# Performance work log

Measured on AMD Instinct MI355X. Metric: run time of the kernel, lower is better.

The kernel has to match this reference:

```python
import jax, jax.numpy as jnp
import numpy as np

B, S, H, E, I_E, V = 4, 4096, 1024, 8, 512, 100000


def setup_inputs() -> dict:
    key = jax.random.key(0)
    k0, k1, k2, k3, k4, k5, k6 = jax.random.split(key, 7)
    hidden_states = jax.random.normal(k0, (B, S, H), dtype=jnp.float32)
    token_ids = jax.random.randint(k1, (B, S), 0, V, dtype=jnp.int64)
    mu = jax.random.normal(k2, (B, S, H), dtype=jnp.float32)
    # torch Linear(in,out,bias=False) weight is [out,in]; we store transposed [in,out]
    w_gate = jax.random.normal(k3, (E, H, I_E), dtype=jnp.float32) * 0.02
    w_up = jax.random.normal(k4, (E, H, I_E), dtype=jnp.float32) * 0.02
    w_down = jax.random.normal(k5, (E, I_E, H), dtype=jnp.float32) * 0.02
    # module zero-inits mu_router; use small random so the mu-override path is exercised
    mu_router_w = jax.random.normal(k6, (E, H), dtype=jnp.float32) * 0.02
    return {
        "hidden_states": hidden_states,
        "token_ids": token_ids,
        "mu": mu,
        "w_gate": w_gate,
        "w_up": w_up,
        "w_down": w_down,
        "mu_router_w": mu_router_w,
    }


def reference(hidden_states, token_ids, mu, w_gate, w_up, w_down, mu_router_w):
    num_experts = w_gate.shape[0]
    # deterministic token->expert mapping: token_id % num_experts (after clamp)
    tid = jnp.clip(token_ids, 0, V - 1)
    base_expert_ids = (tid % num_experts).astype(jnp.int32)  # [B,S]
    # mu-guided override: one_hot*10 + mu_logits, argmax
    mu_logits = jnp.einsum("bsh,eh->bse", mu, mu_router_w)
    base_one_hot = jax.nn.one_hot(base_expert_ids, num_experts, dtype=mu_logits.dtype)
    expert_ids = jnp.argmax(base_one_hot * 10.0 + mu_logits, axis=-1)  # [B,S]

    x = hidden_states.reshape(-1, H)          # [T,H], T=B*S
    eid = expert_ids.reshape(-1)              # [T]
    out = jnp.zeros_like(x)
    for e in range(num_experts):
        mask = (eid == e)[:, None]            # [T,1]
        g = x @ w_gate[e]                     # [T,I_E]
        u = x @ w_up[e]                       # [T,I_E]
        y = (jax.nn.silu(g) * u) @ w_down[e]  # [T,H] SwiGLU
        out = out + jnp.where(mask, y, 0.0)
    return out.reshape(hidden_states.shape)
```

## Files before the change

kernel.cpp:

```cpp
#include <hip/hip_runtime.h>
#include <stdint.h>

#define T_TOK   16384
#define H_DIM   1024
#define IE_DIM  512
#define E_NUM   8
#define V_MAX   100000

typedef __attribute__((ext_vector_type(8))) short bf16x8;
typedef __attribute__((ext_vector_type(4))) float f32x4;
typedef unsigned long long ull;

__device__ __forceinline__ unsigned short f2bf(float f) {
  union { float f; unsigned u; } v; v.f = f;
  unsigned r = v.u + 0x7fffu + ((v.u >> 16) & 1u);
  return (unsigned short)(r >> 16);
}

__device__ __forceinline__ void gload16(const void* g, void* l) {
  __builtin_amdgcn_global_load_lds(
      (const __attribute__((address_space(1))) unsigned int*)g,
      (__attribute__((address_space(3))) unsigned int*)(unsigned int)(uintptr_t)l,
      16, 0, 0);
}

__global__ __launch_bounds__(256) void k_pre(
    const float* __restrict__ mu, const int* __restrict__ tok,
    const float* __restrict__ mrw, int* __restrict__ eid,
    int* __restrict__ blockCnt,
    const float* __restrict__ wg, const float* __restrict__ wu,
    const float* __restrict__ wd, unsigned short* __restrict__ WgT,
    unsigned short* __restrict__ WuT, unsigned short* __restrict__ WdT) {
  __shared__ unsigned short lds[64][72];
  int tid = threadIdx.x;

  if (blockIdx.x < 1024) {
    int* cnt = (int*)&lds[0][0];
    if (tid < 8) cnt[tid] = 0;
    int wv = blockIdx.x * 4 + (tid >> 6);
    int t0 = wv * 4;
    int lane = tid & 63;
    const float4* mrw4 = (const float4*)mrw;

    float acc[4][E_NUM];
#pragma unroll
    for (int i = 0; i < 4; i++)
#pragma unroll
      for (int e = 0; e < E_NUM; e++) acc[i][e] = 0.f;

#pragma unroll
    for (int j = 0; j < 4; j++) {
      int idx = lane + 64 * j;
      float4 wr[E_NUM];
#pragma unroll
      for (int e = 0; e < E_NUM; e++) wr[e] = mrw4[e * 256 + idx];
#pragma unroll
      for (int i = 0; i < 4; i++) {
        float4 m = ((const float4*)(mu + (size_t)(t0 + i) * H_DIM))[idx];
#pragma unroll
        for (int e = 0; e < E_NUM; e++)
          acc[i][e] += m.x * wr[e].x + m.y * wr[e].y + m.z * wr[e].z + m.w * wr[e].w;
      }
    }
#pragma unroll
    for (int i = 0; i < 4; i++)
#pragma unroll
      for (int e = 0; e < E_NUM; e++)
#pragma unroll
        for (int off = 32; off >= 1; off >>= 1)
          acc[i][e] += __shfl_xor(acc[i][e], off, 64);

    __syncthreads();
#pragma unroll
    for (int i = 0; i < 4; i++) {
      int tv = tok[t0 + i];
      if (tv < 0) tv = 0;
      if (tv > V_MAX - 1) tv = V_MAX - 1;
      int base = tv & 7;
      int best = 0; float bs = -1e30f;
#pragma unroll
      for (int e = 0; e < E_NUM; e++) {
        float s = acc[i][e] + (e == base ? 10.f : 0.f);
        if (s > bs) { bs = s; best = e; }
      }
      if (lane == i) {
        eid[t0 + i] = best;
        atomicAdd(&cnt[best], 1);
      }
    }
    __syncthreads();
    if (tid < 8) blockCnt[blockIdx.x * 8 + tid] = cnt[tid];
  } else {
    int sel = (blockIdx.x - 1024) >> 10;
    int blk = blockIdx.x & 1023;
    const float* src; unsigned short* dst; int R, C;
    if (sel == 0)      { src = wg; dst = WgT; R = H_DIM; C = IE_DIM; }
    else if (sel == 1) { src = wu; dst = WuT; R = H_DIM; C = IE_DIM; }
    else               { src = wd; dst = WdT; R = IE_DIM; C = H_DIM; }
    int tpe = (R >> 6) * (C >> 6);
    int e = blk / tpe;
    int rem = blk % tpe;
    int tr = rem / (C >> 6);
    int tc = rem % (C >> 6);
    const float* s = src + (size_t)e * R * C;
    unsigned short* d = dst + (size_t)e * R * C;
    int r0 = tid >> 4;
    int c0 = (tid & 15) * 4;
#pragma unroll
    for (int i = 0; i < 4; i++) {
      int r = r0 + i * 16;
      float4 v = *(const float4*)(s + (size_t)(tr * 64 + r) * C + tc * 64 + c0);
      lds[r][c0 + 0] = f2bf(v.x); lds[r][c0 + 1] = f2bf(v.y);
      lds[r][c0 + 2] = f2bf(v.z); lds[r][c0 + 3] = f2bf(v.w);
    }
    __syncthreads();
    int oc = tid >> 2;
    int ob = (tid & 3) * 16;
    unsigned short tmp[16];
#pragma unroll
    for (int i = 0; i < 16; i++) tmp[i] = lds[ob + i][oc];
    uint4* dp = (uint4*)(d + (size_t)(tc * 64 + oc) * R + tr * 64 + ob);
    dp[0] = ((uint4*)tmp)[0];
    dp[1] = ((uint4*)tmp)[1];
  }
}

__global__ __launch_bounds__(1024) void k_scan2(
    const int* __restrict__ blockCnt, int* __restrict__ blockBase,
    int* __restrict__ offsets, int* __restrict__ tileOff) {
  int b = threadIdx.x;
  __shared__ ull s0[1024], s1[1024];
  __shared__ int offL[8];
  const int4* p = (const int4*)(blockCnt + b * 8);
  int4 x0 = p[0], x1 = p[1];
  int c[8] = {x0.x, x0.y, x0.z, x0.w, x1.x, x1.y, x1.z, x1.w};
  ull v0 = (ull)c[0] | ((ull)c[1] << 16) | ((ull)c[2] << 32) | ((ull)c[3] << 48);
  ull v1 = (ull)c[4] | ((ull)c[5] << 16) | ((ull)c[6] << 32) | ((ull)c[7] << 48);
  s0[b] = v0; s1[b] = v1;
  __syncthreads();
  for (int st = 1; st < 1024; st <<= 1) {
    ull a0 = 0, a1 = 0;
    if (b >= st) { a0 = s0[b - st]; a1 = s1[b - st]; }
    __syncthreads();
    v0 += a0; v1 += a1;
    s0[b] = v0; s1[b] = v1;
    __syncthreads();
  }
  if (b == 1023) {
    int tot[8];
#pragma unroll
    for (int e = 0; e < 4; e++) tot[e] = (int)((v0 >> (16 * e)) & 0xFFFF);
#pragma unroll
    for (int e = 0; e < 4; e++) tot[4 + e] = (int)((v1 >> (16 * e)) & 0xFFFF);
    int s = 0, ts = 0;
    for (int e = 0; e < E_NUM; e++) {
      offsets[e] = s; offL[e] = s; tileOff[e] = ts;
      s += tot[e];
      ts += (tot[e] + 127) >> 7;
    }
    offsets[E_NUM] = s; tileOff[E_NUM] = ts;
  }
  __syncthreads();
  int be[8];
#pragma unroll
  for (int e = 0; e < 4; e++)
    be[e] = offL[e] + (int)((v0 >> (16 * e)) & 0xFFFF) - c[e];
#pragma unroll
  for (int e = 0; e < 4; e++)
    be[4 + e] = offL[4 + e] + (int)((v1 >> (16 * e)) & 0xFFFF) - c[4 + e];
  int4* q = (int4*)(blockBase + b * 8);
  q[0] = make_int4(be[0], be[1], be[2], be[3]);
  q[1] = make_int4(be[4], be[5], be[6], be[7]);
}

__global__ __launch_bounds__(256) void k_gather(
    const float* __restrict__ hs, const int* __restrict__ eid,
    const int* __restrict__ blockBase, int* __restrict__ tokofrow,
    unsigned short* __restrict__ Xs) {
  int b = blockIdx.x;
  int tid = threadIdx.x;
  __shared__ int eL[16];
  __shared__ int posL[16];
  if (tid < 16) eL[tid] = eid[b * 16 + tid];
  __syncthreads();
  if (tid < 16) {
    int e = eL[tid];
    int r = 0;
    for (int j = 0; j < tid; j++) r += (eL[j] == e);
    int pos = blockBase[b * 8 + e] + r;
    posL[tid] = pos;
    tokofrow[pos] = b * 16 + tid;
  }
  __syncthreads();
  int w = tid >> 6, lane = tid & 63;
#pragma unroll
  for (int i = 0; i < 4; i++) {
    int li = w * 4 + i;
    int t = b * 16 + li;
    int pos = posL[li];
    const float4* src = (const float4*)(hs + (size_t)t * H_DIM);
    unsigned short* drow = Xs + (size_t)pos * H_DIM;
#pragma unroll
    for (int j = 0; j < 4; j++) {
      float4 v = src[lane + 64 * j];
      ushort4 bb;
      bb.x = f2bf(v.x); bb.y = f2bf(v.y); bb.z = f2bf(v.z); bb.w = f2bf(v.w);
      *(ushort4*)(drow + (lane + 64 * j) * 4) = bb;
    }
  }
}

__global__ __launch_bounds__(512) void k_gemm1(
    const unsigned short* __restrict__ Xs,
    const unsigned short* __restrict__ WgT,
    const unsigned short* __restrict__ WuT,
    unsigned short* __restrict__ Hb,
    const int* __restrict__ offsets, const int* __restrict__ tileOff) {
  int bid0 = blockIdx.x;
  int xcd = bid0 & 7, seq = bid0 >> 3;
  int wg = (xcd < 4 ? xcd * 68 : 272 + (xcd - 4) * 67) + seq;
  int nt = wg & 3;
  int mlin = wg >> 2;
  if (mlin >= tileOff[E_NUM]) return;
  int e = 0;
#pragma unroll
  for (int i = 1; i < E_NUM; i++)
    if (mlin >= tileOff[i]) e = i;
  int mtile = mlin - tileOff[e];
  int segStart = offsets[e], segEnd = offsets[e + 1];
  int M = segEnd - segStart;

  __shared__ unsigned short Alds[3][128 * 32];
  __shared__ unsigned short Bglds[3][128 * 32];
  __shared__ unsigned short Bulds[3][128 * 32];

  int tid = threadIdx.x;
  int lane = tid & 63;
  int w = tid >> 6;
  int wm = w >> 2;
  int wn = w & 3;

  f32x4 accg[4][2], accu[4][2];
#pragma unroll
  for (int i = 0; i < 4; i++)
#pragma unroll
    for (int j = 0; j < 2; j++) {
      accg[i][j] = (f32x4)(0.f);
      accu[i][j] = (f32x4)(0.f);
    }

  int sr = tid >> 2;
  int sc = tid & 3;
  int scc = sc ^ ((sr >> 1) & 3);
  int grow = mtile * 128 + sr;
  if (grow > M - 1) grow = M - 1;
  const unsigned short* Arow = Xs + (size_t)(segStart + grow) * H_DIM + scc * 8;
  const unsigned short* Bgrow =
      WgT + (size_t)e * IE_DIM * H_DIM + (size_t)(nt * 128 + sr) * H_DIM + scc * 8;
  const unsigned short* Burow =
      WuT + (size_t)e * IE_DIM * H_DIM + (size_t)(nt * 128 + sr) * H_DIM + scc * 8;

#define STAGE1(buf, k0)                                            \
  {                                                                \
    gload16(Arow + (k0), (char*)Alds[buf] + tid * 16);             \
    gload16(Bgrow + (k0), (char*)Bglds[buf] + tid * 16);           \
    gload16(Burow + (k0), (char*)Bulds[buf] + tid * 16);           \
  }

  int kc = lane >> 4;
  int arow[4], browv[2];
#pragma unroll
  for (int mf = 0; mf < 4; mf++) arow[mf] = wm * 64 + mf * 16 + (lane & 15);
#pragma unroll
  for (int nf = 0; nf < 2; nf++) browv[nf] = wn * 32 + nf * 16 + (lane & 15);

  const int NT = H_DIM / 32;
  STAGE1(0, 0);
  STAGE1(1, 32);

  int cur = 0;
  for (int t = 0; t < NT; t++) {
    asm volatile("s_waitcnt vmcnt(3)" ::: "memory");
    __builtin_amdgcn_s_barrier();
    __builtin_amdgcn_sched_barrier(0);
    int tn = t + 2; if (tn >= NT) tn -= NT;
    int nbuf = cur + 2; if (nbuf >= 3) nbuf -= 3;
    STAGE1(nbuf, tn * 32);

    bf16x8 a[4], bg[2], bu[2];
#pragma unroll
    for (int mf = 0; mf < 4; mf++) {
      int row = arow[mf];
      int byte = row * 64 + ((kc ^ ((row >> 1) & 3)) << 4);
      a[mf] = *(const bf16x8*)((const char*)Alds[cur] + byte);
    }
#pragma unroll
    for (int nf = 0; nf < 2; nf++) {
      int row = browv[nf];
      int byte = row * 64 + ((kc ^ ((row >> 1) & 3)) << 4);
      bg[nf] = *(const bf16x8*)((const char*)Bglds[cur] + byte);
      bu[nf] = *(const bf16x8*)((const char*)Bulds[cur] + byte);
    }
    __builtin_amdgcn_s_setprio(1);
#pragma unroll
    for (int mf = 0; mf < 4; mf++)
#pragma unroll
      for (int nf = 0; nf < 2; nf++) {
        accg[mf][nf] = __builtin_amdgcn_mfma_f32_16x16x32_bf16(
            a[mf], bg[nf], accg[mf][nf], 0, 0, 0);
        accu[mf][nf] = __builtin_amdgcn_mfma_f32_16x16x32_bf16(
            a[mf], bu[nf], accu[mf][nf], 0, 0, 0);
      }
    __builtin_amdgcn_s_setprio(0);
    cur = (cur + 1 == 3) ? 0 : cur + 1;
  }
#undef STAGE1
  asm volatile("s_waitcnt vmcnt(0)" ::: "memory");

  int rowBase = segStart + mtile * 128 + wm * 64;
#pragma unroll
  for (int mf = 0; mf < 4; mf++)
#pragma unroll
    for (int nf = 0; nf < 2; nf++) {
      int col = nt * 128 + wn * 32 + nf * 16 + (lane & 15);
#pragma unroll
      for (int j = 0; j < 4; j++) {
        int r = rowBase + mf * 16 + (lane >> 4) * 4 + j;
        if (r < segEnd) {
          float g = accg[mf][nf][j];
          float u = accu[mf][nf][j];
          float h = (g / (1.f + __expf(-g))) * u;
          Hb[(size_t)r * IE_DIM + col] = f2bf(h);
        }
      }
    }
}

__global__ __launch_bounds__(512) void k_gemm2(
    const unsigned short* __restrict__ Hb,
    const unsigned short* __restrict__ WdT,
    float* __restrict__ out,
    const int* __restrict__ offsets, const int* __restrict__ tileOff,
    const int* __restrict__ tokofrow) {
  int bid0 = blockIdx.x;
  int wg = (bid0 & 7) * 135 + (bid0 >> 3);
  int nt = wg & 7;
  int mlin = wg >> 3;
  if (mlin >= tileOff[E_NUM]) return;
  int e = 0;
#pragma unroll
  for (int i = 1; i < E_NUM; i++)
    if (mlin >= tileOff[i]) e = i;
  int mtile = mlin - tileOff[e];
  int segStart = offsets[e], segEnd = offsets[e + 1];
  int M = segEnd - segStart;

  __shared__ unsigned short Alds[3][128 * 32];
  __shared__ unsigned short Blds[3][128 * 32];

  int tid = threadIdx.x;
  int lane = tid & 63;
  int w = tid >> 6;
  int wm = w >> 2;
  int wn = w & 3;

  f32x4 acc[4][2];
#pragma unroll
  for (int i = 0; i < 4; i++)
#pragma unroll
    for (int j = 0; j < 2; j++) acc[i][j] = (f32x4)(0.f);

  int sr = tid >> 2;
  int sc = tid & 3;
  int scc = sc ^ ((sr >> 1) & 3);
  int grow = mtile * 128 + sr;
  if (grow > M - 1) grow = M - 1;
  const unsigned short* Arow = Hb + (size_t)(segStart + grow) * IE_DIM + scc * 8;
  const unsigned short* Brow =
      WdT + (size_t)e * H_DIM * IE_DIM + (size_t)(nt * 128 + sr) * IE_DIM + scc * 8;

#define STAGE2(buf, k0)                                            \
  {                                                                \
    gload16(Arow + (k0), (char*)Alds[buf] + tid * 16);             \
    gload16(Brow + (k0), (char*)Blds[buf] + tid * 16);             \
  }

  int kc = lane >> 4;
  int arow[4], browv[2];
#pragma unroll
  for (int mf = 0; mf < 4; mf++) arow[mf] = wm * 64 + mf * 16 + (lane & 15);
#pragma unroll
  for (int nf = 0; nf < 2; nf++) browv[nf] = wn * 32 + nf * 16 + (lane & 15);

  const int NT = IE_DIM / 32;
  STAGE2(0, 0);
  STAGE2(1, 32);

  int cur = 0;
  for (int t = 0; t < NT; t++) {
    asm volatile("s_waitcnt vmcnt(2)" ::: "memory");
    __builtin_amdgcn_s_barrier();
    __builtin_amdgcn_sched_barrier(0);
    int tn = t + 2; if (tn >= NT) tn -= NT;
    int nbuf = cur + 2; if (nbuf >= 3) nbuf -= 3;
    STAGE2(nbuf, tn * 32);

    bf16x8 a[4], b[2];
#pragma unroll
    for (int mf = 0; mf < 4; mf++) {
      int row = arow[mf];
      int byte = row * 64 + ((kc ^ ((row >> 1) & 3)) << 4);
      a[mf] = *(const bf16x8*)((const char*)Alds[cur] + byte);
    }
#pragma unroll
    for (int nf = 0; nf < 2; nf++) {
      int row = browv[nf];
      int byte = row * 64 + ((kc ^ ((row >> 1) & 3)) << 4);
      b[nf] = *(const bf16x8*)((const char*)Blds[cur] + byte);
    }
    __builtin_amdgcn_s_setprio(1);
#pragma unroll
    for (int mf = 0; mf < 4; mf++)
#pragma unroll
      for (int nf = 0; nf < 2; nf++)
        acc[mf][nf] = __builtin_amdgcn_mfma_f32_16x16x32_bf16(
            a[mf], b[nf], acc[mf][nf], 0, 0, 0);
    __builtin_amdgcn_s_setprio(0);
    cur = (cur + 1 == 3) ? 0 : cur + 1;
  }
#undef STAGE2
  asm volatile("s_waitcnt vmcnt(0)" ::: "memory");

  int rowBase = segStart + mtile * 128 + wm * 64;
#pragma unroll
  for (int mf = 0; mf < 4; mf++)
#pragma unroll
    for (int nf = 0; nf < 2; nf++) {
      int col = nt * 128 + wn * 32 + nf * 16 + (lane & 15);
#pragma unroll
      for (int j = 0; j < 4; j++) {
        int r = rowBase + mf * 16 + (lane >> 4) * 4 + j;
        if (r < segEnd) {
          int t = tokofrow[r];
          out[(size_t)t * H_DIM + col] = acc[mf][nf][j];
        }
      }
    }
}

#define WS_XS    ((size_t)0)
#define WS_WGT   ((size_t)33554432)
#define WS_WUT   ((size_t)41943040)
#define WS_WDT   ((size_t)50331648)
#define WS_HB    ((size_t)58720256)
#define WS_EID   ((size_t)75497472)
#define WS_TOK   ((size_t)75563008)
#define WS_OFF   ((size_t)75628544)
#define WS_BC    ((size_t)75629568)
#define WS_BB    ((size_t)75662336)

extern "C" void kernel_launch(void* const* d_in, const int* in_sizes, int n_in,
                              void* d_out, int out_size, void* d_ws, size_t ws_size,
                              hipStream_t stream) {
  const float* hs  = (const float*)d_in[0];
  const int*   tok = (const int*)d_in[1];
  const float* mu  = (const float*)d_in[2];
  const float* wg  = (const float*)d_in[3];
  const float* wu  = (const float*)d_in[4];
  const float* wd  = (const float*)d_in[5];
  const float* mrw = (const float*)d_in[6];
  float* out = (float*)d_out;
  char* ws = (char*)d_ws;

  unsigned short* Xs  = (unsigned short*)(ws + WS_XS);
  unsigned short* WgT = (unsigned short*)(ws + WS_WGT);
  unsigned short* WuT = (unsigned short*)(ws + WS_WUT);
  unsigned short* WdT = (unsigned short*)(ws + WS_WDT);
  unsigned short* Hb  = (unsigned short*)(ws + WS_HB);
  int* eid      = (int*)(ws + WS_EID);
  int* tokofrow = (int*)(ws + WS_TOK);
  int* offsets  = (int*)(ws + WS_OFF);
  int* tileOff  = offsets + 16;
  int* blockCnt = (int*)(ws + WS_BC);
  int* blockBase= (int*)(ws + WS_BB);

  k_pre<<<4096, 256, 0, stream>>>(mu, tok, mrw, eid, blockCnt,
                                  wg, wu, wd, WgT, WuT, WdT);
  k_scan2<<<1, 1024, 0, stream>>>(blockCnt, blockBase, offsets, tileOff);
  k_gather<<<1024, 256, 0, stream>>>(hs, eid, blockBase, tokofrow, Xs);
  k_gemm1<<<135 * 4, 512, 0, stream>>>(Xs, WgT, WuT, Hb, offsets, tileOff);
  k_gemm2<<<135 * 8, 512, 0, stream>>>(Hb, WdT, out, offsets, tileOff, tokofrow);
}
```

Measured before the change: 155.8 us.

## Enlarge gemm1 tiles to 256x128 with K=64 double-buffered staging

Rewrites the fused gate/up GEMM kernel to use 256-row M tiles and a 64-wide K step with two LDS buffers instead of three 32-wide ones. Each wave now computes a 64x64 block for both gate and up, which raises MFMA work per LDS load and halves the loop trip count. The scan kernel now emits separate 256-row tile offsets for gemm1 and 128-row offsets for gemm2, and the XCD remapping and grid size are adjusted to match. The cost is much higher register and LDS use, so occupancy drops to one block per CU. Fewer blocks also means more padding waste on partial expert tiles.

```diff
diff --git a/kernel.cpp b/kernel.cpp
--- a/kernel.cpp
+++ b/kernel.cpp
@@ -127,7 +127,8 @@
 
 __global__ __launch_bounds__(1024) void k_scan2(
     const int* __restrict__ blockCnt, int* __restrict__ blockBase,
-    int* __restrict__ offsets, int* __restrict__ tileOff) {
+    int* __restrict__ offsets, int* __restrict__ tileOff,
+    int* __restrict__ tileOff128) {
   int b = threadIdx.x;
   __shared__ ull s0[1024], s1[1024];
   __shared__ int offL[8];
@@ -152,13 +153,15 @@
     for (int e = 0; e < 4; e++) tot[e] = (int)((v0 >> (16 * e)) & 0xFFFF);
 #pragma unroll
     for (int e = 0; e < 4; e++) tot[4 + e] = (int)((v1 >> (16 * e)) & 0xFFFF);
-    int s = 0, ts = 0;
+    int s = 0, ts = 0, ts2 = 0;
     for (int e = 0; e < E_NUM; e++) {
-      offsets[e] = s; offL[e] = s; tileOff[e] = ts;
+      offsets[e] = s; offL[e] = s;
+      tileOff[e] = ts; tileOff128[e] = ts2;
       s += tot[e];
-      ts += (tot[e] + 127) >> 7;
-    }
-    offsets[E_NUM] = s; tileOff[E_NUM] = ts;
+      ts += (tot[e] + 255) >> 8;
+      ts2 += (tot[e] + 127) >> 7;
+    }
+    offsets[E_NUM] = s; tileOff[E_NUM] = ts; tileOff128[E_NUM] = ts2;
   }
   __syncthreads();
   int be[8];
@@ -210,7 +213,7 @@
   }
 }
 
-__global__ __launch_bounds__(512) void k_gemm1(
+__global__ __launch_bounds__(512, 1) void k_gemm1(
     const unsigned short* __restrict__ Xs,
     const unsigned short* __restrict__ WgT,
     const unsigned short* __restrict__ WuT,
@@ -218,7 +221,7 @@
     const int* __restrict__ offsets, const int* __restrict__ tileOff) {
   int bid0 = blockIdx.x;
   int xcd = bid0 & 7, seq = bid0 >> 3;
-  int wg = (xcd < 4 ? xcd * 68 : 272 + (xcd - 4) * 67) + seq;
+  int wg = (xcd < 4 ? xcd * 36 : 144 + (xcd - 4) * 35) + seq;
   int nt = wg & 3;
   int mlin = wg >> 2;
   if (mlin >= tileOff[E_NUM]) return;
@@ -230,99 +233,171 @@
   int segStart = offsets[e], segEnd = offsets[e + 1];
   int M = segEnd - segStart;
 
-  __shared__ unsigned short Alds[3][128 * 32];
-  __shared__ unsigned short Bglds[3][128 * 32];
-  __shared__ unsigned short Bulds[3][128 * 32];
+  __shared__ unsigned short Alds[2][256 * 64];
+  __shared__ unsigned short Bglds[2][128 * 64];
+  __shared__ unsigned short Bulds[2][128 * 64];
 
   int tid = threadIdx.x;
   int lane = tid & 63;
   int w = tid >> 6;
-  int wm = w >> 2;
-  int wn = w & 3;
-
-  f32x4 accg[4][2], accu[4][2];
+  int wm = w >> 1;
+  int wn = w & 1;
+  int r0 = lane & 15;
+  int kcb = lane >> 4;
+
+  f32x4 accg[4][4], accu[4][4];
 #pragma unroll
   for (int i = 0; i < 4; i++)
 #pragma unroll
-    for (int j = 0; j < 2; j++) {
+    for (int j = 0; j < 4; j++) {
       accg[i][j] = (f32x4)(0.f);
       accu[i][j] = (f32x4)(0.f);
     }
 
-  int sr = tid >> 2;
-  int sc = tid & 3;
-  int scc = sc ^ ((sr >> 1) & 3);
-  int grow = mtile * 128 + sr;
-  if (grow > M - 1) grow = M - 1;
-  const unsigned short* Arow = Xs + (size_t)(segStart + grow) * H_DIM + scc * 8;
-  const unsigned short* Bgrow =
-      WgT + (size_t)e * IE_DIM * H_DIM + (size_t)(nt * 128 + sr) * H_DIM + scc * 8;
-  const unsigned short* Burow =
-      WuT + (size_t)e * IE_DIM * H_DIM + (size_t)(nt * 128 + sr) * H_DIM + scc * 8;
-
-#define STAGE1(buf, k0)                                            \
-  {                                                                \
-    gload16(Arow + (k0), (char*)Alds[buf] + tid * 16);             \
-    gload16(Bgrow + (k0), (char*)Bglds[buf] + tid * 16);           \
-    gload16(Burow + (k0), (char*)Bulds[buf] + tid * 16);           \
-  }
-
-  int kc = lane >> 4;
-  int arow[4], browv[2];
-#pragma unroll
-  for (int mf = 0; mf < 4; mf++) arow[mf] = wm * 64 + mf * 16 + (lane & 15);
-#pragma unroll
-  for (int nf = 0; nf < 2; nf++) browv[nf] = wn * 32 + nf * 16 + (lane & 15);
-
-  const int NT = H_DIM / 32;
-  STAGE1(0, 0);
-  STAGE1(1, 32);
-
-  int cur = 0;
-  for (int t = 0; t < NT; t++) {
-    asm volatile("s_waitcnt vmcnt(3)" ::: "memory");
+  const unsigned short* Asrc[4];
+#pragma unroll
+  for (int i = 0; i < 4; i++) {
+    int s = tid + i * 512;
+    int row = s >> 3;
+    int ch = (s & 7) ^ (row & 7);
+    int gr = mtile * 256 + row; if (gr > M - 1) gr = M - 1;
+    Asrc[i] = Xs + (size_t)(segStart + gr) * H_DIM + ch * 8;
+  }
+  const unsigned short* Bgsrc[2];
+  const unsigned short* Busrc[2];
+#pragma unroll
+  for (int i = 0; i < 2; i++) {
+    int s = tid + i * 512;
+    int row = s >> 3;
+    int ch = (s & 7) ^ (row & 7);
+    Bgsrc[i] = WgT + (size_t)e * IE_DIM * H_DIM + (size_t)(nt * 128 + row) * H_DIM + ch * 8;
+    Busrc[i] = WuT + (size_t)e * IE_DIM * H_DIM + (size_t)(nt * 128 + row) * H_DIM + ch * 8;
+  }
+
+#define GLA(i, kt, buf) gload16(Asrc[i] + (kt) * 64, (char*)Alds[buf] + (tid + (i) * 512) * 16)
+#define GLG(i, kt, buf) gload16(Bgsrc[i] + (kt) * 64, (char*)Bglds[buf] + (tid + (i) * 512) * 16)
+#define GLU(i, kt, buf) gload16(Busrc[i] + (kt) * 64, (char*)Bulds[buf] + (tid + (i) * 512) * 16)
+
+  int aoff[4][2], boff[4][2];
+#pragma unroll
+  for (int mf = 0; mf < 4; mf++) {
+    int row = wm * 64 + mf * 16 + r0;
+#pragma unroll
+    for (int ks = 0; ks < 2; ks++) {
+      int c = ks * 4 + kcb;
+      aoff[mf][ks] = row * 128 + ((c ^ (row & 7)) << 4);
+    }
+  }
+#pragma unroll
+  for (int nf = 0; nf < 4; nf++) {
+    int row = wn * 64 + nf * 16 + r0;
+#pragma unroll
+    for (int ks = 0; ks < 2; ks++) {
+      int c = ks * 4 + kcb;
+      boff[nf][ks] = row * 128 + ((c ^ (row & 7)) << 4);
+    }
+  }
+
+  const int NT = H_DIM / 64;
+  GLA(0, 0, 0); GLA(1, 0, 0); GLA(2, 0, 0); GLA(3, 0, 0);
+  GLG(0, 0, 0); GLG(1, 0, 0); GLU(0, 0, 0); GLU(1, 0, 0);
+
+  bf16x8 a0[2][2], a1[2][2], bb[4][2];
+
+  for (int kt = 0; kt < NT; kt++) {
+    int buf = kt & 1, nbuf = buf ^ 1;
+    int ktn = (kt + 1 < NT) ? kt + 1 : 0;
+    const char* Ab = (const char*)Alds[buf];
+    const char* Bgb = (const char*)Bglds[buf];
+    const char* Bub = (const char*)Bulds[buf];
+
     __builtin_amdgcn_s_barrier();
+    GLA(0, ktn, nbuf); GLA(1, ktn, nbuf); GLA(2, ktn, nbuf); GLA(3, ktn, nbuf);
+    GLG(0, ktn, nbuf); GLG(1, ktn, nbuf); GLU(0, ktn, nbuf); GLU(1, ktn, nbuf);
+    asm volatile("s_waitcnt vmcnt(8)" ::: "memory");
+    __builtin_amdgcn_s_barrier();
+
+#pragma unroll
+    for (int mf = 0; mf < 2; mf++)
+#pragma unroll
+      for (int ks = 0; ks < 2; ks++)
+        a0[mf][ks] = *(const bf16x8*)(Ab + aoff[mf][ks]);
+#pragma unroll
+    for (int nf = 0; nf < 4; nf++)
+#pragma unroll
+      for (int ks = 0; ks < 2; ks++)
+        bb[nf][ks] = *(const bf16x8*)(Bgb + boff[nf][ks]);
+    asm volatile("s_waitcnt lgkmcnt(0)" ::: "memory");
     __builtin_amdgcn_sched_barrier(0);
-    int tn = t + 2; if (tn >= NT) tn -= NT;
-    int nbuf = cur + 2; if (nbuf >= 3) nbuf -= 3;
-    STAGE1(nbuf, tn * 32);
-
-    bf16x8 a[4], bg[2], bu[2];
-#pragma unroll
-    for (int mf = 0; mf < 4; mf++) {
-      int row = arow[mf];
-      int byte = row * 64 + ((kc ^ ((row >> 1) & 3)) << 4);
-      a[mf] = *(const bf16x8*)((const char*)Alds[cur] + byte);
-    }
-#pragma unroll
-    for (int nf = 0; nf < 2; nf++) {
-      int row = browv[nf];
-      int byte = row * 64 + ((kc ^ ((row >> 1) & 3)) << 4);
-      bg[nf] = *(const bf16x8*)((const char*)Bglds[cur] + byte);
-      bu[nf] = *(const bf16x8*)((const char*)Bulds[cur] + byte);
-    }
     __builtin_amdgcn_s_setprio(1);
 #pragma unroll
-    for (int mf = 0; mf < 4; mf++)
-#pragma unroll
-      for (int nf = 0; nf < 2; nf++) {
-        accg[mf][nf] = __builtin_amdgcn_mfma_f32_16x16x32_bf16(
-            a[mf], bg[nf], accg[mf][nf], 0, 0, 0);
-        accu[mf][nf] = __builtin_amdgcn_mfma_f32_16x16x32_bf16(
-            a[mf], bu[nf], accu[mf][nf], 0, 0, 0);
-      }
+    for (int mf = 0; mf < 2; mf++)
+#pragma unroll
+      for (int nf = 0; nf < 4; nf++)
+#pragma unroll
+        for (int ks = 0; ks < 2; ks++)
+          accg[mf][nf] = __builtin_amdgcn_mfma_f32_16x16x32_bf16(
+              a0[mf][ks], bb[nf][ks], accg[mf][nf], 0, 0, 0);
     __builtin_amdgcn_s_setprio(0);
-    cur = (cur + 1 == 3) ? 0 : cur + 1;
-  }
-#undef STAGE1
+
+#pragma unroll
+    for (int mf = 0; mf < 2; mf++)
+#pragma unroll
+      for (int ks = 0; ks < 2; ks++)
+        a1[mf][ks] = *(const bf16x8*)(Ab + aoff[2 + mf][ks]);
+    asm volatile("s_waitcnt lgkmcnt(0)" ::: "memory");
+    __builtin_amdgcn_sched_barrier(0);
+    __builtin_amdgcn_s_setprio(1);
+#pragma unroll
+    for (int mf = 0; mf < 2; mf++)
+#pragma unroll
+      for (int nf = 0; nf < 4; nf++)
+#pragma unroll
+        for (int ks = 0; ks < 2; ks++)
+          accg[2 + mf][nf] = __builtin_amdgcn_mfma_f32_16x16x32_bf16(
+              a1[mf][ks], bb[nf][ks], accg[2 + mf][nf], 0, 0, 0);
+    __builtin_amdgcn_s_setprio(0);
+
+#pragma unroll
+    for (int nf = 0; nf < 4; nf++)
+#pragma unroll
+      for (int ks = 0; ks < 2; ks++)
+        bb[nf][ks] = *(const bf16x8*)(Bub + boff[nf][ks]);
+    asm volatile("s_waitcnt lgkmcnt(0)" ::: "memory");
+    __builtin_amdgcn_sched_barrier(0);
+    __builtin_amdgcn_s_setprio(1);
+#pragma unroll
+    for (int mf = 0; mf < 2; mf++)
+#pragma unroll
+      for (int nf = 0; nf < 4; nf++)
+#pragma unroll
+        for (int ks = 0; ks < 2; ks++)
+          accu[mf][nf] = __builtin_amdgcn_mfma_f32_16x16x32_bf16(
+              a0[mf][ks], bb[nf][ks], accu[mf][nf], 0, 0, 0);
+    __builtin_amdgcn_s_setprio(0);
+
+    __builtin_amdgcn_s_setprio(1);
+#pragma unroll
+    for (int mf = 0; mf < 2; mf++)
+#pragma unroll
+      for (int nf = 0; nf < 4; nf++)
+#pragma unroll
+        for (int ks = 0; ks < 2; ks++)
+          accu[2 + mf][nf] = __builtin_amdgcn_mfma_f32_16x16x32_bf16(
+              a1[mf][ks], bb[nf][ks], accu[2 + mf][nf], 0, 0, 0);
+    __builtin_amdgcn_s_setprio(0);
+  }
   asm volatile("s_waitcnt vmcnt(0)" ::: "memory");
-
-  int rowBase = segStart + mtile * 128 + wm * 64;
+#undef GLA
+#undef GLG
+#undef GLU
+
+  int rowBase = segStart + mtile * 256 + wm * 64;
 #pragma unroll
   for (int mf = 0; mf < 4; mf++)
 #pragma unroll
-    for (int nf = 0; nf < 2; nf++) {
-      int col = nt * 128 + wn * 32 + nf * 16 + (lane & 15);
+    for (int nf = 0; nf < 4; nf++) {
+      int col = nt * 128 + wn * 64 + nf * 16 + r0;
 #pragma unroll
       for (int j = 0; j < 4; j++) {
         int r = rowBase + mf * 16 + (lane >> 4) * 4 + j;
@@ -479,15 +554,16 @@
   unsigned short* Hb  = (unsigned short*)(ws + WS_HB);
   int* eid      = (int*)(ws + WS_EID);
   int* tokofrow = (int*)(ws + WS_TOK);
-  int* offsets  = (int*)(ws + WS_OFF);
-  int* tileOff  = offsets + 16;
+  int* offsets   = (int*)(ws + WS_OFF);
+  int* tileOff   = offsets + 16;
+  int* tileOff128= offsets + 32;
   int* blockCnt = (int*)(ws + WS_BC);
   int* blockBase= (int*)(ws + WS_BB);
 
   k_pre<<<4096, 256, 0, stream>>>(mu, tok, mrw, eid, blockCnt,
                                   wg, wu, wd, WgT, WuT, WdT);
-  k_scan2<<<1, 1024, 0, stream>>>(blockCnt, blockBase, offsets, tileOff);
+  k_scan2<<<1, 1024, 0, stream>>>(blockCnt, blockBase, offsets, tileOff, tileOff128);
   k_gather<<<1024, 256, 0, stream>>>(hs, eid, blockBase, tokofrow, Xs);
-  k_gemm1<<<135 * 4, 512, 0, stream>>>(Xs, WgT, WuT, Hb, offsets, tileOff);
-  k_gemm2<<<135 * 8, 512, 0, stream>>>(Hb, WdT, out, offsets, tileOff, tokofrow);
-}
+  k_gemm1<<<284, 512, 0, stream>>>(Xs, WgT, WuT, Hb, offsets, tileOff);
+  k_gemm2<<<135 * 8, 512, 0, stream>>>(Hb, WdT, out, offsets, tileOff128, tokofrow);
+}
```

Result: slower. 169.0 us (+8.5%).
